# Optimization experiments

Measured on AMD Instinct MI355X. Metric: run time of the kernel, lower is better.

Reference implementation:

```python
import jax, jax.numpy as jnp
import numpy as np

EPS = 1e-16


def setup_inputs() -> dict:
    key = jax.random.key(0)
    ks = jax.random.split(key, 8)
    B, C, F, H = 524288, 10, 10, 8  # batch, clusters, feats/cluster, tail hidden
    HC = 8  # head hidden = ceil(10 * 0.75)
    return {
        "x": jax.random.uniform(ks[0], (B, C * F), dtype=jnp.float32),
        "tail_enc_w": jax.random.normal(ks[1], (C, H, F), dtype=jnp.float32) * 0.3,
        "tail_enc_b": jax.random.normal(ks[2], (C, H), dtype=jnp.float32) * 0.1,
        "tail_dec_w": jax.random.normal(ks[3], (C, F, H), dtype=jnp.float32) * 0.3,
        "tail_dec_b": jax.random.normal(ks[4], (C, F), dtype=jnp.float32) * 0.1,
        "tail_nmin": jnp.zeros((C, F), dtype=jnp.float32),
        "tail_nmax": jnp.ones((C, F), dtype=jnp.float32),
        "head_enc_w": jax.random.normal(ks[5], (HC, C), dtype=jnp.float32) * 0.3,
        "head_enc_b": jax.random.normal(ks[6], (HC,), dtype=jnp.float32) * 0.1,
        "head_dec_w": jax.random.normal(ks[7], (C, HC), dtype=jnp.float32) * 0.3,
        "head_dec_b": jnp.zeros((C,), dtype=jnp.float32),
        "head_nmin": jnp.zeros((C,), dtype=jnp.float32),
        "head_nmax": jnp.ones((C,), dtype=jnp.float32),
    }


def reference(x, tail_enc_w, tail_enc_b, tail_dec_w, tail_dec_b,
              tail_nmin, tail_nmax, head_enc_w, head_enc_b,
              head_dec_w, head_dec_b, head_nmin, head_nmax):
    B = x.shape[0]
    C, H, F = tail_enc_w.shape
    # split the 100 features into C contiguous clusters of size F: [B, C, F]
    xc = x.reshape(B, C, F)
    # per-tail min-max normalisation (BaseAutoencoder.normalise)
    xn = (xc - tail_nmin) / (tail_nmax - tail_nmin + EPS)
    # all tails batched into one grouped matmul (sigmoid(Linear) twice)
    h = jax.nn.sigmoid(jnp.einsum('bcf,chf->bch', xn, tail_enc_w) + tail_enc_b)
    rec = jax.nn.sigmoid(jnp.einsum('bch,cfh->bcf', h, tail_dec_w) + tail_dec_b)
    # RMSE per (packet, cluster); infer mode => no log
    loss = jnp.sqrt(jnp.mean((rec - xn) ** 2, axis=-1))  # [B, C]
    tails = jnp.where(loss == 0, jnp.float32(0.01), loss)
    # head-level min-max normalisation (Kitsune.normalise)
    t = (tails - head_nmin) / (head_nmax - head_nmin + EPS)
    hh = jax.nn.sigmoid(t @ head_enc_w.T + head_enc_b)
    x_hat = jax.nn.sigmoid(hh @ head_dec_w.T + head_dec_b)
    return x_hat, t
```

## Files before the change

### kernel.cpp

```cpp
#include <hip/hip_runtime.h>

#define KEPS  1e-16f
#define LOG2E 1.44269504088896340736f

typedef float v2f __attribute__((ext_vector_type(2)));


__global__ void kitsune_prep(
    const float* __restrict__ tew, const float* __restrict__ teb,
    const float* __restrict__ tdw, const float* __restrict__ tdb,
    const float* __restrict__ tnmin, const float* __restrict__ tnmax,
    const float* __restrict__ hew, const float* __restrict__ heb,
    const float* __restrict__ hdw, const float* __restrict__ hdb,
    const float* __restrict__ hnmin, const float* __restrict__ hnmax,
    float* __restrict__ ws)
{
    const int i = threadIdx.x;
    for (int k = i; k < 100; k += 256) {
        float s = 1.0f / (tnmax[k] - tnmin[k] + KEPS);
        ws[k]        = s;
        ws[100 + k]  = -tnmin[k] * s;
        ws[1880 + k] = tdb[k] * -LOG2E;
    }
    for (int k = i; k < 800; k += 256) {
        ws[200 + k]  = tew[k] * -LOG2E;
        ws[1080 + k] = tdw[k] * -LOG2E;
    }
    for (int k = i; k < 80; k += 256) {
        ws[1000 + k] = teb[k] * -LOG2E;
        ws[2000 + k] = hew[k] * -LOG2E;
        ws[2088 + k] = hdw[k] * -LOG2E;
    }
    if (i < 10) {
        float s = 1.0f / (hnmax[i] - hnmin[i] + KEPS);
        ws[1980 + i] = s;
        ws[1990 + i] = -hnmin[i] * s;
        ws[2168 + i] = hdb[i] * -LOG2E;
    }
    if (i < 8) ws[2080 + i] = heb[i] * -LOG2E;
}

__device__ __forceinline__ float sig2(float a) {
    return __builtin_amdgcn_rcpf(1.0f + __builtin_amdgcn_exp2f(a));
}

__global__ __launch_bounds__(640) void kitsune_main(
    const float* __restrict__ x,
    const float* __restrict__ ws,
    float* __restrict__ out_xhat,
    float* __restrict__ out_t,
    int B)
{
    __shared__ float xs[64 * 102];
    __shared__ float ts[64 * 11];
    __shared__ float hs[64 * 9];
    __shared__ float os[64 * 11];

    const int tid  = threadIdx.x;
    const int base = (int)blockIdx.x * 64;
    const int rows = min(64, B - base);
    const int n25  = rows * 25;

    {
        const float4* gx = reinterpret_cast<const float4*>(x) + (size_t)base * 25;
        #pragma unroll
        for (int n = 0; n < 3; ++n) {
            int idx = tid + n * 640;
            if (idx < n25) {
                float4 v = gx[idx];
                int row = idx / 25;
                int q   = idx - row * 25;
                float* d = xs + row * 102 + q * 4;
                *reinterpret_cast<float2*>(d)     = make_float2(v.x, v.y);
                *reinterpret_cast<float2*>(d + 2) = make_float2(v.z, v.w);
            }
        }
    }
    __syncthreads();

    {
        const int c = __builtin_amdgcn_readfirstlane(tid >> 6);
        const int r = tid & 63;

        v2f xp[5];
        #pragma unroll
        for (int j = 0; j < 5; ++j)
            xp[j] = *reinterpret_cast<const v2f*>(xs + r * 102 + c * 10 + 2 * j);

        const v2f* sc2 = reinterpret_cast<const v2f*>(ws + c * 10);
        const v2f* bi2 = reinterpret_cast<const v2f*>(ws + 100 + c * 10);
        #pragma unroll
        for (int j = 0; j < 5; ++j)
            xp[j] = __builtin_elementwise_fma(xp[j], sc2[j], bi2[j]);

        v2f hv[4];
        #pragma unroll
        for (int i = 0; i < 8; ++i) {
            const v2f* w2 = reinterpret_cast<const v2f*>(ws + 200 + (c * 8 + i) * 10);
            v2f a2 = w2[0] * xp[0];
            #pragma unroll
            for (int j = 1; j < 5; ++j)
                a2 = __builtin_elementwise_fma(w2[j], xp[j], a2);
            hv[i >> 1][i & 1] = sig2(ws[1000 + c * 8 + i] + a2.x + a2.y);
        }

        v2f ss2 = {0.0f, 0.0f};
        float dprev = 0.0f;
        #pragma unroll
        for (int f = 0; f < 10; ++f) {
            const v2f* w2 = reinterpret_cast<const v2f*>(ws + 1080 + (c * 10 + f) * 8);
            v2f a2 = w2[0] * hv[0];
            #pragma unroll
            for (int i = 1; i < 4; ++i)
                a2 = __builtin_elementwise_fma(w2[i], hv[i], a2);
            float rec = sig2(ws[1880 + c * 10 + f] + a2.x + a2.y);
            float d   = rec - xp[f >> 1][f & 1];
            if (f & 1) {
                v2f d2 = {dprev, d};
                ss2 = __builtin_elementwise_fma(d2, d2, ss2);
            } else {
                dprev = d;
            }
        }
        float l    = __builtin_amdgcn_sqrtf((ss2.x + ss2.y) * 0.1f);
        float tail = (l == 0.0f) ? 0.01f : l;
        ts[r * 11 + c] = fmaf(tail, ws[1980 + c], ws[1990 + c]);
    }
    __syncthreads();

    if (tid < 512) {
        const int i = __builtin_amdgcn_readfirstlane(tid >> 6);
        const int r = tid & 63;
        float a = ws[2080 + i];
        #pragma unroll
        for (int cc = 0; cc < 10; ++cc)
            a = fmaf(ws[2000 + i * 10 + cc], ts[r * 11 + cc], a);
        hs[r * 9 + i] = sig2(a);
    }
    __syncthreads();

    {
        const int c = __builtin_amdgcn_readfirstlane(tid >> 6);
        const int r = tid & 63;
        float a = ws[2168 + c];
        #pragma unroll
        for (int i = 0; i < 8; ++i)
            a = fmaf(ws[2088 + c * 8 + i], hs[r * 9 + i], a);
        os[r * 11 + c] = sig2(a);
    }
    __syncthreads();

    if (tid < 320) {
        int row = tid / 5, j = tid - row * 5;
        if (row < rows) {
            float2 v = make_float2(ts[row * 11 + 2 * j], ts[row * 11 + 2 * j + 1]);
            *reinterpret_cast<float2*>(out_t + (size_t)(base + row) * 10 + 2 * j) = v;
        }
    } else {
        int q   = tid - 320;
        int row = q / 5, j = q - row * 5;
        if (row < rows) {
            float2 v = make_float2(os[row * 11 + 2 * j], os[row * 11 + 2 * j + 1]);
            *reinterpret_cast<float2*>(out_xhat + (size_t)(base + row) * 10 + 2 * j) = v;
        }
    }
}

extern "C" void kernel_launch(void* const* d_in, const int* in_sizes, int n_in,
                              void* d_out, int out_size, void* d_ws, size_t ws_size,
                              hipStream_t stream) {
    const float* x          = (const float*)d_in[0];
    const float* tail_enc_w = (const float*)d_in[1];
    const float* tail_enc_b = (const float*)d_in[2];
    const float* tail_dec_w = (const float*)d_in[3];
    const float* tail_dec_b = (const float*)d_in[4];
    const float* tail_nmin  = (const float*)d_in[5];
    const float* tail_nmax  = (const float*)d_in[6];
    const float* head_enc_w = (const float*)d_in[7];
    const float* head_enc_b = (const float*)d_in[8];
    const float* head_dec_w = (const float*)d_in[9];
    const float* head_dec_b = (const float*)d_in[10];
    const float* head_nmin  = (const float*)d_in[11];
    const float* head_nmax  = (const float*)d_in[12];

    const int B = in_sizes[0] / 100;

    float* out_xhat = (float*)d_out;
    float* out_t    = out_xhat + (size_t)B * 10;
    float* ws       = (float*)d_ws;

    kitsune_prep<<<1, 256, 0, stream>>>(
        tail_enc_w, tail_enc_b, tail_dec_w, tail_dec_b, tail_nmin, tail_nmax,
        head_enc_w, head_enc_b, head_dec_w, head_dec_b, head_nmin, head_nmax, ws);

    const int grid = (B + 63) / 64;
    kitsune_main<<<grid, 640, 0, stream>>>(x, ws, out_xhat, out_t, B);
}
```

Measured before the change: 77.09 us.

## Split fused kernel into tail and head kernels with 320-thread tail blocks

Splits the single fused kernel into two. The tail kernel uses 320 threads per block, each handling two clusters, and writes normalised tail losses straight to global memory. A separate per-row head kernel then reads them back to compute the head autoencoder, which removes the extra shared-memory stages and barriers. In exchange it adds a second launch plus a global write and reread of t, and the tail kernel's per-column strided stores are uncoalesced.

```diff
diff --git a/kernel.cpp b/kernel.cpp
--- a/kernel.cpp
+++ b/kernel.cpp
@@ -44,17 +44,13 @@
     return __builtin_amdgcn_rcpf(1.0f + __builtin_amdgcn_exp2f(a));
 }
 
-__global__ __launch_bounds__(640) void kitsune_main(
+__global__ __launch_bounds__(320) void kitsune_tail(
     const float* __restrict__ x,
     const float* __restrict__ ws,
-    float* __restrict__ out_xhat,
     float* __restrict__ out_t,
     int B)
 {
     __shared__ float xs[64 * 102];
-    __shared__ float ts[64 * 11];
-    __shared__ float hs[64 * 9];
-    __shared__ float os[64 * 11];
 
     const int tid  = threadIdx.x;
     const int base = (int)blockIdx.x * 64;
@@ -64,8 +60,8 @@
     {
         const float4* gx = reinterpret_cast<const float4*>(x) + (size_t)base * 25;
         #pragma unroll
-        for (int n = 0; n < 3; ++n) {
-            int idx = tid + n * 640;
+        for (int n = 0; n < 5; ++n) {
+            int idx = tid + n * 320;
             if (idx < n25) {
                 float4 v = gx[idx];
                 int row = idx / 25;
@@ -78,9 +74,11 @@
     }
     __syncthreads();
 
-    {
-        const int c = __builtin_amdgcn_readfirstlane(tid >> 6);
-        const int r = tid & 63;
+    const int r = tid & 63;
+
+    #pragma unroll
+    for (int k = 0; k < 2; ++k) {
+        const int c = __builtin_amdgcn_readfirstlane((tid >> 6) + 5 * k);
 
         v2f xp[5];
         #pragma unroll
@@ -124,46 +122,55 @@
         }
         float l    = __builtin_amdgcn_sqrtf((ss2.x + ss2.y) * 0.1f);
         float tail = (l == 0.0f) ? 0.01f : l;
-        ts[r * 11 + c] = fmaf(tail, ws[1980 + c], ws[1990 + c]);
-    }
-    __syncthreads();
-
-    if (tid < 512) {
-        const int i = __builtin_amdgcn_readfirstlane(tid >> 6);
-        const int r = tid & 63;
-        float a = ws[2080 + i];
-        #pragma unroll
-        for (int cc = 0; cc < 10; ++cc)
-            a = fmaf(ws[2000 + i * 10 + cc], ts[r * 11 + cc], a);
-        hs[r * 9 + i] = sig2(a);
-    }
-    __syncthreads();
-
+        float tv   = fmaf(tail, ws[1980 + c], ws[1990 + c]);
+
+        if (r < rows)
+            out_t[(size_t)(base + r) * 10 + c] = tv;
+    }
+}
+
+__global__ __launch_bounds__(256) void kitsune_head(
+    const float* __restrict__ t_in,
+    const float* __restrict__ ws,
+    float* __restrict__ out_xhat,
+    int B)
+{
+    const int b = blockIdx.x * 256 + threadIdx.x;
+    if (b >= B) return;
+
+    v2f tp[5];
     {
-        const int c = __builtin_amdgcn_readfirstlane(tid >> 6);
-        const int r = tid & 63;
-        float a = ws[2168 + c];
-        #pragma unroll
-        for (int i = 0; i < 8; ++i)
-            a = fmaf(ws[2088 + c * 8 + i], hs[r * 9 + i], a);
-        os[r * 11 + c] = sig2(a);
-    }
-    __syncthreads();
-
-    if (tid < 320) {
-        int row = tid / 5, j = tid - row * 5;
-        if (row < rows) {
-            float2 v = make_float2(ts[row * 11 + 2 * j], ts[row * 11 + 2 * j + 1]);
-            *reinterpret_cast<float2*>(out_t + (size_t)(base + row) * 10 + 2 * j) = v;
-        }
-    } else {
-        int q   = tid - 320;
-        int row = q / 5, j = q - row * 5;
-        if (row < rows) {
-            float2 v = make_float2(os[row * 11 + 2 * j], os[row * 11 + 2 * j + 1]);
-            *reinterpret_cast<float2*>(out_xhat + (size_t)(base + row) * 10 + 2 * j) = v;
-        }
-    }
+        const v2f* tr = reinterpret_cast<const v2f*>(t_in + (size_t)b * 10);
+        #pragma unroll
+        for (int j = 0; j < 5; ++j) tp[j] = tr[j];
+    }
+
+    v2f hv[4];
+    #pragma unroll
+    for (int i = 0; i < 8; ++i) {
+        const v2f* w2 = reinterpret_cast<const v2f*>(ws + 2000 + i * 10);
+        v2f a2 = w2[0] * tp[0];
+        #pragma unroll
+        for (int j = 1; j < 5; ++j)
+            a2 = __builtin_elementwise_fma(w2[j], tp[j], a2);
+        hv[i >> 1][i & 1] = sig2(ws[2080 + i] + a2.x + a2.y);
+    }
+
+    float xh[10];
+    #pragma unroll
+    for (int c = 0; c < 10; ++c) {
+        const v2f* w2 = reinterpret_cast<const v2f*>(ws + 2088 + c * 8);
+        v2f a2 = w2[0] * hv[0];
+        #pragma unroll
+        for (int i = 1; i < 4; ++i)
+            a2 = __builtin_elementwise_fma(w2[i], hv[i], a2);
+        xh[c] = sig2(ws[2168 + c] + a2.x + a2.y);
+    }
+
+    float* po = out_xhat + (size_t)b * 10;
+    #pragma unroll
+    for (int j = 0; j < 5; ++j)
+        *reinterpret_cast<float2*>(po + 2 * j) = make_float2(xh[2 * j], xh[2 * j + 1]);
 }
 
 extern "C" void kernel_launch(void* const* d_in, const int* in_sizes, int n_in,
@@ -193,6 +200,9 @@
         tail_enc_w, tail_enc_b, tail_dec_w, tail_dec_b, tail_nmin, tail_nmax,
         head_enc_w, head_enc_b, head_dec_w, head_dec_b, head_nmin, head_nmax, ws);
 
-    const int grid = (B + 63) / 64;
-    kitsune_main<<<grid, 640, 0, stream>>>(x, ws, out_xhat, out_t, B);
-}
+    const int gridA = (B + 63) / 64;
+    kitsune_tail<<<gridA, 320, 0, stream>>>(x, ws, out_t, B);
+
+    const int gridB = (B + 255) / 256;
+    kitsune_head<<<gridB, 256, 0, stream>>>(out_t, ws, out_xhat, B);
+}
```

Measured after the change: 72.07 us. 6.5% less time.
